# Optimization experiments

Hardware: AMD Instinct MI355X
Metric: run time of the kernel (lower is better)

The kernel has to match this reference:

```python
import jax, jax.numpy as jnp
import numpy as np

HID = 128          # args.hid
HEADS = 1          # args.head (forced: concat=True and classifier expects 3*hid)
C = HID            # out_channels per head
ND, NPR, NCL = 4096, 20000, 1024
E_DD, E_DP, E_CP = 500_000, 1_000_000, 500_000
B = 8192
SLOPE = 0.2        # GATConv negative_slope default


def _gat(x_src, x_dst, src, dst, W, a_src, a_dst, bias, num_dst,
         edge_attr=None, W_edge=None, a_edge=None):
    # PyG GATConv: shared lin for src/dst (in_channels is int)
    hs = (x_src @ W).reshape(-1, HEADS, C)            # [Ns,H,C]
    hd = (x_dst @ W).reshape(-1, HEADS, C)            # [Nd,H,C]
    e = jnp.sum(hs * a_src, -1)[src] + jnp.sum(hd * a_dst, -1)[dst]  # [E,H]
    if edge_attr is not None:
        ee = (edge_attr @ W_edge).reshape(-1, HEADS, C)
        e = e + jnp.sum(ee * a_edge, -1)
    e = jnp.where(e > 0, e, SLOPE * e)                # leaky_relu
    emax = jax.ops.segment_max(e, dst, num_segments=num_dst)
    ex = jnp.exp(e - emax[dst])
    denom = jax.ops.segment_sum(ex, dst, num_segments=num_dst)
    alpha = ex / (denom[dst] + 1e-16)                 # PyG softmax eps
    out = jax.ops.segment_sum(hs[src] * alpha[:, :, None], dst, num_segments=num_dst)
    return out.reshape(num_dst, HEADS * C) + bias


def _l2n(x):
    return x / jnp.maximum(jnp.linalg.norm(x, axis=1, keepdims=True), 1e-12)


def setup_inputs() -> dict:
    key = jax.random.key(0)
    ks = iter(jax.random.split(key, 48))

    def nrm(shape, s=0.1):
        return jax.random.normal(next(ks), shape, jnp.float32) * s

    inp = {
        'x_drug': jnp.arange(ND, dtype=jnp.int32),
        'x_protein': jnp.arange(NPR, dtype=jnp.int32),
        'x_cell': jnp.arange(NCL, dtype=jnp.int32),
        'ei_dd': jax.random.randint(next(ks), (2, E_DD), 0, ND),
        'edge_attr_dd': jax.random.normal(next(ks), (E_DD, 1), jnp.float32),
        'src_dp': jax.random.randint(next(ks), (E_DP,), 0, NPR),
        'dst_dp': jax.random.randint(next(ks), (E_DP,), 0, ND),
        'src_cp': jax.random.randint(next(ks), (E_CP,), 0, NPR),
        'dst_cp': jax.random.randint(next(ks), (E_CP,), 0, NCL),
        'drug1': jax.random.randint(next(ks), (B,), 0, ND),
        'drug2': jax.random.randint(next(ks), (B,), 0, ND),
        'cell': jax.random.randint(next(ks), (B,), 0, NCL),
        # embedding tables
        'drug_emb': nrm((ND, HID), 1.0),
        'protein_emb': nrm((NPR, HID), 1.0),
        'cell_emb': nrm((NCL, HID), 1.0),
        # GAT d-d (edge_dim=1)
        'W_dd': nrm((HID, HEADS * C)), 'a_src_dd': nrm((HEADS, C)), 'a_dst_dd': nrm((HEADS, C)),
        'bias_dd': jnp.zeros((HEADS * C,), jnp.float32),
        'W_edge_dd': nrm((1, HEADS * C)), 'a_edge_dd': nrm((HEADS, C)),
        # GAT protein->drug
        'W_dp': nrm((HID, HEADS * C)), 'a_src_dp': nrm((HEADS, C)), 'a_dst_dp': nrm((HEADS, C)),
        'bias_dp': jnp.zeros((HEADS * C,), jnp.float32),
        # GAT protein->cell
        'W_cp': nrm((HID, HEADS * C)), 'a_src_cp': nrm((HEADS, C)), 'a_dst_cp': nrm((HEADS, C)),
        'bias_cp': jnp.zeros((HEADS * C,), jnp.float32),
        # classifier: 3h -> 6h -> 2h -> 2
        'W1': nrm((3 * HID, 6 * HID)), 'b1': jnp.zeros((6 * HID,), jnp.float32),
        'W2': nrm((6 * HID, 2 * HID)), 'b2': jnp.zeros((2 * HID,), jnp.float32),
        'W3': nrm((2 * HID, 2)), 'b3': jnp.zeros((2,), jnp.float32),
    }
    return inp


def reference(x_drug, x_protein, x_cell, ei_dd, edge_attr_dd, src_dp, dst_dp,
              src_cp, dst_cp, drug1, drug2, cell, drug_emb, protein_emb, cell_emb,
              W_dd, a_src_dd, a_dst_dd, bias_dd, W_edge_dd, a_edge_dd,
              W_dp, a_src_dp, a_dst_dp, bias_dp,
              W_cp, a_src_cp, a_dst_cp, bias_cp,
              W1, b1, W2, b2, W3, b3):
    h_d = drug_emb[x_drug]
    h_p = protein_emb[x_protein]
    h_c = cell_emb[x_cell]

    # d-d: add self-loops with edge_attr fill_value='mean' (PyG default)
    src, dst = ei_dd[0], ei_dd[1]
    deg = jax.ops.segment_sum(jnp.ones((E_DD,), jnp.float32), dst, num_segments=ND)
    mean_attr = jax.ops.segment_sum(edge_attr_dd, dst, num_segments=ND) / jnp.maximum(deg, 1.0)[:, None]
    loops = jnp.arange(ND, dtype=src.dtype)
    src2 = jnp.concatenate([src, loops])
    dst2 = jnp.concatenate([dst, loops])
    attr2 = jnp.concatenate([edge_attr_dd, mean_attr], 0)

    out_dd = _gat(h_d, h_d, src2, dst2, W_dd, a_src_dd, a_dst_dd, bias_dd, ND,
                  attr2, W_edge_dd, a_edge_dd)
    out_dp = _gat(h_p, h_d, src_dp, dst_dp, W_dp, a_src_dp, a_dst_dp, bias_dp, ND)
    out_cp = _gat(h_p, h_c, src_cp, dst_cp, W_cp, a_src_cp, a_dst_cp, bias_cp, NCL)

    drug = jax.nn.relu(out_dd + out_dp)   # HeteroConv aggr='sum', then F.relu
    cellx = jax.nn.relu(out_cp)

    hid = jnp.concatenate([_l2n(drug[drug1]), _l2n(drug[drug2]), _l2n(cellx[cell])], 1)
    h = jax.nn.relu(hid @ W1 + b1)        # dropout = identity in eval
    h = jax.nn.relu(h @ W2 + b2)
    return h @ W3 + b3
```

## Files before the change

### kernel.cpp

```cpp
#include <hip/hip_runtime.h>
#include <hip/hip_bf16.h>

#define HIDC 128
typedef __hip_bfloat16 bf16;
typedef __attribute__((ext_vector_type(8))) short short8;
typedef __attribute__((ext_vector_type(4))) float floatx4;

#define CHUNK 4096

__device__ __forceinline__ short f2b(float f) {
    unsigned int u = __builtin_bit_cast(unsigned int, f);
    u += 0x7fff + ((u >> 16) & 1);
    return (short)(u >> 16);
}

__device__ __forceinline__ uint packe(int s, float ev) {
    float w = __expf(ev);
    return ((uint)s << 16) | (uint)(unsigned short)f2b(w);
}

__global__ void __launch_bounds__(256) r11_prep(
    int* __restrict__ zptr, int zwords, int nzb,
    const float* __restrict__ W_dd, const float* __restrict__ W_dp, const float* __restrict__ W_cp,
    const float* __restrict__ a0, const float* __restrict__ a1, const float* __restrict__ a2,
    const float* __restrict__ a3, const float* __restrict__ a4, const float* __restrict__ a5,
    const float* __restrict__ W_edge, const float* __restrict__ a_edge,
    float* __restrict__ wa, float* __restrict__ c_edge,
    const float* __restrict__ W1, short* __restrict__ Wt1, int nT1,
    const float* __restrict__ W2, short* __restrict__ Wt2)
{
    int b = blockIdx.x;
    int tid = threadIdx.x;
    if (b < nzb) {
        int i = b * 256 + tid;
        if (i < zwords) zptr[i] = 0;
        return;
    }
    b -= nzb;
    if (b < 7) {
        __shared__ float as[HIDC];
        int k = tid;
        if (b < 6) {
            const float* W = (b < 2) ? W_dd : (b < 4) ? W_dp : W_cp;
            const float* a = (b == 0) ? a0 : (b == 1) ? a1 : (b == 2) ? a2 : (b == 3) ? a3 : (b == 4) ? a4 : a5;
            if (k < HIDC) as[k] = a[k];
            __syncthreads();
            if (k < HIDC) {
                float s = 0.f;
#pragma unroll 8
                for (int c = 0; c < HIDC; c++) s = fmaf(W[k * HIDC + c], as[c], s);
                wa[b * HIDC + k] = s;
            }
        } else {
            if (k < HIDC) as[k] = W_edge[k] * a_edge[k];
            __syncthreads();
#pragma unroll
            for (int off = 64; off > 0; off >>= 1) { if (k < off) as[k] += as[k + off]; __syncthreads(); }
            if (k == 0) c_edge[0] = as[0];
        }
        return;
    }
    b -= 7;
    const float* W; short* Wt; int K, N, k0, n0;
    if (b < nT1) { W = W1; Wt = Wt1; K = 384; N = 768; k0 = (b / 24) * 32; n0 = (b % 24) * 32; }
    else { b -= nT1; W = W2; Wt = Wt2; K = 768; N = 256; k0 = (b / 8) * 32; n0 = (b % 8) * 32; }
    __shared__ short T[32 * 34];
    int cc = tid & 31, rr = tid >> 5;
#pragma unroll
    for (int it = 0; it < 4; it++) {
        int r = it * 8 + rr;
        T[r * 34 + cc] = f2b(W[(size_t)(k0 + r) * N + n0 + cc]);
    }
    __syncthreads();
#pragma unroll
    for (int it = 0; it < 4; it++) {
        int r = it * 8 + rr;
        Wt[(size_t)(n0 + r) * K + k0 + cc] = T[cc * 34 + r];
    }
}

__global__ void __launch_bounds__(256) r11_scalars(
    const float* __restrict__ drug_emb, const float* __restrict__ prot_emb, const float* __restrict__ cell_emb,
    const int* __restrict__ x_drug, const int* __restrict__ x_prot, const int* __restrict__ x_cell,
    const float* __restrict__ wa,
    float* __restrict__ ssrc_dd, float* __restrict__ sdst_dd, float* __restrict__ sdst_dp,
    float* __restrict__ ssrc_dp, float* __restrict__ ssrc_cp, float* __restrict__ sdst_cp,
    int nd, int npr, int ncl)
{
    int g = blockIdx.x * 4 + (threadIdx.x >> 6);
    int l = threadIdx.x & 63;
    const float2* wa2 = (const float2*)wa;
    if (g < nd) {
        int id = x_drug[g];
        float2 e = ((const float2*)drug_emb)[(size_t)id * 64 + l];
        float2 w0 = wa2[0 * 64 + l], w1 = wa2[1 * 64 + l], w3 = wa2[3 * 64 + l];
        float p0 = e.x * w0.x + e.y * w0.y;
        float p1 = e.x * w1.x + e.y * w1.y;
        float p2 = e.x * w3.x + e.y * w3.y;
#pragma unroll
        for (int off = 32; off > 0; off >>= 1) {
            p0 += __shfl_xor(p0, off, 64);
            p1 += __shfl_xor(p1, off, 64);
            p2 += __shfl_xor(p2, off, 64);
        }
        if (l == 0) { ssrc_dd[g] = p0; sdst_dd[g] = p1; sdst_dp[g] = p2; }
    } else if (g < nd + npr) {
        int r = g - nd;
        int id = x_prot[r];
        float2 e = ((const float2*)prot_emb)[(size_t)id * 64 + l];
        float2 w2 = wa2[2 * 64 + l], w4 = wa2[4 * 64 + l];
        float p0 = e.x * w2.x + e.y * w2.y;
        float p1 = e.x * w4.x + e.y * w4.y;
#pragma unroll
        for (int off = 32; off > 0; off >>= 1) {
            p0 += __shfl_xor(p0, off, 64);
            p1 += __shfl_xor(p1, off, 64);
        }
        if (l == 0) { ssrc_dp[r] = p0; ssrc_cp[r] = p1; }
    } else if (g < nd + npr + ncl) {
        int r = g - nd - npr;
        int id = x_cell[r];
        float2 e = ((const float2*)cell_emb)[(size_t)id * 64 + l];
        float2 w5 = wa2[5 * 64 + l];
        float p0 = e.x * w5.x + e.y * w5.y;
#pragma unroll
        for (int off = 32; off > 0; off >>= 1) p0 += __shfl_xor(p0, off, 64);
        if (l == 0) sdst_cp[r] = p0;
    }
}

__global__ void __launch_bounds__(128) r11_node_gemm(
    const float* __restrict__ drug_emb, const int* __restrict__ x_drug,
    const float* __restrict__ W_dd, bf16* __restrict__ H_dd, int ndb,
    const float* __restrict__ prot_emb, const int* __restrict__ x_prot,
    const float* __restrict__ W_dp, const float* __restrict__ W_cp,
    bf16* __restrict__ H_dp, bf16* __restrict__ H_cp)
{
    __shared__ int ids[16];
    __shared__ float xs[16 * HIDC];
    int bb = blockIdx.x;
    bool isdrug = bb < ndb;
    int r0 = (isdrug ? bb : bb - ndb) * 16;
    const float* emb = isdrug ? drug_emb : prot_emb;
    const int* idx = isdrug ? x_drug : x_prot;
    int tid = threadIdx.x;
    if (tid < 16) ids[tid] = idx[r0 + tid];
    __syncthreads();
    for (int t = tid; t < 16 * HIDC; t += 128) {
        int r = t >> 7, k = t & 127;
        xs[t] = emb[(size_t)ids[r] * HIDC + k];
    }
    __syncthreads();
    int c = tid;
    if (isdrug) {
        float acc[16];
#pragma unroll
        for (int r = 0; r < 16; r++) acc[r] = 0.f;
        for (int k = 0; k < HIDC; k += 4) {
            float w0 = W_dd[(k + 0) * HIDC + c];
            float w1 = W_dd[(k + 1) * HIDC + c];
            float w2 = W_dd[(k + 2) * HIDC + c];
            float w3 = W_dd[(k + 3) * HIDC + c];
#pragma unroll
            for (int r = 0; r < 16; r++) {
                float4 x = *(const float4*)&xs[r * HIDC + k];
                acc[r] = fmaf(x.x, w0, fmaf(x.y, w1, fmaf(x.z, w2, fmaf(x.w, w3, acc[r]))));
            }
        }
#pragma unroll
        for (int r = 0; r < 16; r++) H_dd[(size_t)(r0 + r) * HIDC + c] = __float2bfloat16(acc[r]);
    } else {
        float accA[16], accB[16];
#pragma unroll
        for (int r = 0; r < 16; r++) { accA[r] = 0.f; accB[r] = 0.f; }
        for (int k = 0; k < HIDC; k += 2) {
            float a0 = W_dp[(k + 0) * HIDC + c];
            float a1 = W_dp[(k + 1) * HIDC + c];
            float b0 = W_cp[(k + 0) * HIDC + c];
            float b1 = W_cp[(k + 1) * HIDC + c];
#pragma unroll
            for (int r = 0; r < 16; r++) {
                float2 x = *(const float2*)&xs[r * HIDC + k];
                accA[r] = fmaf(x.x, a0, fmaf(x.y, a1, accA[r]));
                accB[r] = fmaf(x.x, b0, fmaf(x.y, b1, accB[r]));
            }
        }
#pragma unroll
        for (int r = 0; r < 16; r++) {
            H_dp[(size_t)(r0 + r) * HIDC + c] = __float2bfloat16(accA[r]);
            H_cp[(size_t)(r0 + r) * HIDC + c] = __float2bfloat16(accB[r]);
        }
    }
}

__global__ void __launch_bounds__(256) r11_edge_pass1(
    const int* __restrict__ dst_dd, const float* __restrict__ attr_dd, int E_dd, int nb_dd,
    const int* __restrict__ dst_dp, int E_dp, int nb_dp,
    const int* __restrict__ dst_cp, int E_cp,
    int nd, int ncl,
    int* __restrict__ cnt_dd, float* __restrict__ attr_sum,
    int* __restrict__ cnt_dp, int* __restrict__ cnt_cp,
    int* __restrict__ rank_dd, int* __restrict__ rank_dp, int* __restrict__ rank_cp)
{
    __shared__ int lcnt[4096];
    __shared__ float lattr[4096];
    int bid = blockIdx.x;
    const int* dst; const float* attr = nullptr; int E, e0, bins;
    int* gcnt; int* rank;
    if (bid < nb_dd) {
        dst = dst_dd; attr = attr_dd; E = E_dd; e0 = bid * CHUNK; bins = nd;
        gcnt = cnt_dd; rank = rank_dd;
    } else if (bid < nb_dd + nb_dp) {
        dst = dst_dp; E = E_dp; e0 = (bid - nb_dd) * CHUNK; bins = nd;
        gcnt = cnt_dp; rank = rank_dp;
    } else {
        dst = dst_cp; E = E_cp; e0 = (bid - nb_dd - nb_dp) * CHUNK; bins = ncl;
        gcnt = cnt_cp; rank = rank_cp;
    }
    int tid = threadIdx.x;
    for (int b = tid; b < bins; b += 256) { lcnt[b] = 0; if (attr) lattr[b] = 0.f; }
    __syncthreads();
    int e1 = min(e0 + CHUNK, E);
    for (int i = e0 + tid; i < e1; i += 256) {
        int d = dst[i];
        rank[i] = atomicAdd(&lcnt[d], 1);
        if (attr) atomicAdd(&lattr[d], attr[i]);
    }
    __syncthreads();
    for (int b = tid; b < bins; b += 256) {
        int c = lcnt[b];
        if (c > 0) {
            lcnt[b] = atomicAdd(&gcnt[b], c);
            if (attr) atomicAdd(&attr_sum[b], lattr[b]);
        }
    }
    __syncthreads();
    for (int i = e0 + tid; i < e1; i += 256) {
        rank[i] += lcnt[dst[i]];
    }
}

__global__ void __launch_bounds__(1024) r11_exscan3(
    const int* __restrict__ in0, int* __restrict__ out0, int n0,
    const int* __restrict__ in1, int* __restrict__ out1, int n1,
    const int* __restrict__ in2, int* __restrict__ out2, int n2)
{
    const int* in; int* out; int n; int inc;
    if (blockIdx.x == 0)      { in = in0; out = out0; n = n0; inc = 1; }
    else if (blockIdx.x == 1) { in = in1; out = out1; n = n1; inc = 0; }
    else                      { in = in2; out = out2; n = n2; inc = 0; }
    __shared__ int buf[1024];
    __shared__ int carry;
    int tid = threadIdx.x;
    if (tid == 0) carry = 0;
    __syncthreads();
    for (int base = 0; base < n; base += 1024) {
        int i = base + tid;
        int v = (i < n) ? (in[i] + inc) : 0;
        buf[tid] = v; __syncthreads();
        for (int off = 1; off < 1024; off <<= 1) {
            int t = (tid >= off) ? buf[tid - off] : 0;
            __syncthreads();
            buf[tid] += t;
            __syncthreads();
        }
        int c0 = carry;
        int incl = buf[tid];
        if (i < n) out[i] = c0 + incl - v;
        __syncthreads();
        if (tid == 1023) carry = c0 + buf[1023];
        __syncthreads();
    }
    if (tid == 0) out[n] = carry;
}

__global__ void r11_scatter(
    const int* __restrict__ ei_dd, const float* __restrict__ attr_dd, int E_dd, int nd,
    const int* __restrict__ src_dp, const int* __restrict__ dst_dp, int E_dp,
    const int* __restrict__ src_cp, const int* __restrict__ dst_cp, int E_cp,
    const int* __restrict__ rank_dd, const int* __restrict__ rank_dp, const int* __restrict__ rank_cp,
    const int* __restrict__ deg_dd, const float* __restrict__ attr_sum,
    const float* __restrict__ c_edge_ptr,
    const float* __restrict__ ssrc_dd, const float* __restrict__ sdst_dd,
    const float* __restrict__ ssrc_dp, const float* __restrict__ sdst_dp,
    const float* __restrict__ ssrc_cp, const float* __restrict__ sdst_cp,
    const int* __restrict__ rs_dd, const int* __restrict__ rs_dp, const int* __restrict__ rs_cp,
    uint* __restrict__ csr_dd, uint* __restrict__ csr_dp, uint* __restrict__ csr_cp)
{
    int i = blockIdx.x * 256 + threadIdx.x;
    if (i < E_dd) {
        int s = ei_dd[i], d = ei_dd[E_dd + i];
        float ev = ssrc_dd[s] + sdst_dd[d] + attr_dd[i] * c_edge_ptr[0];
        ev = (ev > 0.f) ? ev : 0.2f * ev;
        csr_dd[rs_dd[d] + rank_dd[i]] = packe(s, ev);
        return;
    }
    i -= E_dd;
    if (i < nd) {
        int d = i;
        int dg = deg_dd[d];
        float mean = attr_sum[d] / fmaxf((float)dg, 1.0f);
        float ev = ssrc_dd[d] + sdst_dd[d] + mean * c_edge_ptr[0];
        ev = (ev > 0.f) ? ev : 0.2f * ev;
        csr_dd[rs_dd[d] + dg] = packe(d, ev);
        return;
    }
    i -= nd;
    if (i < E_dp) {
        int d = dst_dp[i], s = src_dp[i];
        float ev = ssrc_dp[s] + sdst_dp[d];
        ev = (ev > 0.f) ? ev : 0.2f * ev;
        csr_dp[rs_dp[d] + rank_dp[i]] = packe(s, ev);
        return;
    }
    i -= E_dp;
    if (i < E_cp) {
        int d = dst_cp[i], s = src_cp[i];
        float ev = ssrc_cp[s] + sdst_cp[d];
        ev = (ev > 0.f) ? ev : 0.2f * ev;
        csr_cp[rs_cp[d] + rank_cp[i]] = packe(s, ev);
    }
}

__global__ void __launch_bounds__(64) r11_agg3(
    const int* __restrict__ rs_dd, const uint* __restrict__ csr_dd, const uint* __restrict__ Hdd,
    float* __restrict__ agg_dd, int nd,
    const int* __restrict__ rs_dp, const uint* __restrict__ csr_dp, const uint* __restrict__ Hdp,
    float* __restrict__ agg_dp,
    const int* __restrict__ rs_cp, const uint* __restrict__ csr_cp, const uint* __restrict__ Hcp,
    float* __restrict__ agg_cp, int R)
{
    int b = blockIdx.x;
    int slot = b & 7;
    int half = slot >> 2;
    int row_g = (b >> 3) * 4 + (slot & 3);
    if (row_g >= R) return;
    const int* rs; const uint* csr; const uint* H2; float* out; int row;
    if (row_g < nd)          { rs = rs_dd; csr = csr_dd; H2 = Hdd; out = agg_dd; row = row_g; }
    else if (row_g < 2 * nd) { rs = rs_dp; csr = csr_dp; H2 = Hdp; out = agg_dp; row = row_g - nd; }
    else                     { rs = rs_cp; csr = csr_cp; H2 = Hcp; out = agg_cp; row = row_g - 2 * nd; }
    int t = threadIdx.x;
    int c = t & 31, g = t >> 5;
    int s = rs[row], e = rs[row + 1];

    float sum = 0.f;
    for (int i = s + t; i < e; i += 64) sum += __uint_as_float((csr[i] & 0xffffu) << 16);
#pragma unroll
    for (int off = 32; off > 0; off >>= 1) sum += __shfl_xor(sum, off, 64);
    float inv = 1.f / (sum + 1e-16f);

    __shared__ float se[64];
    __shared__ int ss[64];
    const uint* Hh = H2 + half * 32 + c;
    float accx = 0.f, accy = 0.f;
    int base = s;
    for (; base + 64 <= e; base += 64) {
        uint pk = csr[base + t];
        se[t] = __uint_as_float((pk & 0xffffu) << 16);
        ss[t] = (int)(pk >> 16);
        __syncthreads();
#pragma unroll 8
        for (int jj = 0; jj < 32; jj++) {
            int j = jj * 2 + g;
            uint u = Hh[(size_t)ss[j] * 64];
            float w = se[j];
            accx = fmaf(w, __uint_as_float(u << 16), accx);
            accy = fmaf(w, __uint_as_float(u & 0xffff0000u), accy);
        }
        __syncthreads();
    }
    if (base < e) {
        int lim = e - base;
        if (t < lim) {
            uint pk = csr[base + t];
            se[t] = __uint_as_float((pk & 0xffffu) << 16);
            ss[t] = (int)(pk >> 16);
        }
        __syncthreads();
        for (int j = g; j < lim; j += 2) {
            uint u = Hh[(size_t)ss[j] * 64];
            float w = se[j];
            accx = fmaf(w, __uint_as_float(u << 16), accx);
            accy = fmaf(w, __uint_as_float(u & 0xffff0000u), accy);
        }
        __syncthreads();
    }
    accx += __shfl_xor(accx, 32, 64);
    accy += __shfl_xor(accy, 32, 64);
    if (t < 32) {
        float2 o; o.x = accx * inv; o.y = accy * inv;
        ((float2*)out)[(size_t)row * 64 + half * 32 + c] = o;
    }
}

__global__ void __launch_bounds__(128) r11_fuse(
    const float* __restrict__ agg_dd, const float* __restrict__ bias_dd,
    const float* __restrict__ agg_dp, const float* __restrict__ bias_dp,
    float* __restrict__ drugN, int nd,
    const float* __restrict__ agg_cp, const float* __restrict__ bias_cp,
    float* __restrict__ cellN)
{
    int b = blockIdx.x, c = threadIdx.x;
    float v;
    float* outN;
    int d;
    if (b < nd) {
        d = b;
        v = agg_dd[(size_t)d * HIDC + c] + bias_dd[c] + agg_dp[(size_t)d * HIDC + c] + bias_dp[c];
        outN = drugN;
    } else {
        d = b - nd;
        v = agg_cp[(size_t)d * HIDC + c] + bias_cp[c];
        outN = cellN;
    }
    v = fmaxf(v, 0.f);
    __shared__ float red[HIDC];
    red[c] = v * v; __syncthreads();
#pragma unroll
    for (int off = 64; off > 0; off >>= 1) { if (c < off) red[c] += red[c + off]; __syncthreads(); }
    float nrm = fmaxf(sqrtf(red[0]), 1e-12f);
    outN[(size_t)d * HIDC + c] = v / nrm;
}

__global__ void __launch_bounds__(128) r11_gather_hid(
    const float* __restrict__ drugN, const float* __restrict__ cellN,
    const int* __restrict__ d1, const int* __restrict__ d2, const int* __restrict__ ce,
    short* __restrict__ hid)
{
    int b = blockIdx.x, c = threadIdx.x;
    hid[(size_t)b * 384 + c]       = f2b(drugN[(size_t)d1[b] * HIDC + c]);
    hid[(size_t)b * 384 + 128 + c] = f2b(drugN[(size_t)d2[b] * HIDC + c]);
    hid[(size_t)b * 384 + 256 + c] = f2b(cellN[(size_t)ce[b] * HIDC + c]);
}

template <int NB, int OUT_BF16>
__global__ void __launch_bounds__(256) r11_mgemm(
    const short* __restrict__ X, const short* __restrict__ Wt, const float* __restrict__ bias,
    void* __restrict__ Y, int M, int K, int N)
{
    constexpr int BN = NB * 16;
    __shared__ short As[128 * 40];
    __shared__ short Bs[BN * 40];
    int m0 = blockIdx.x * 128, n0 = blockIdx.y * BN;
    int tid = threadIdx.x;
    int w = tid >> 6, lane = tid & 63;
    int q = lane >> 4, t = lane & 15;
    int sr = tid >> 1, sc = tid & 1;

    floatx4 acc[2][NB];
#pragma unroll
    for (int i = 0; i < 2; i++)
#pragma unroll
        for (int c = 0; c < NB; c++) acc[i][c] = (floatx4){0.f, 0.f, 0.f, 0.f};

    for (int kt = 0; kt < K; kt += 32) {
        {
            const uint4* ga = (const uint4*)(X + (size_t)(m0 + sr) * K + kt + sc * 16);
            uint4 a0 = ga[0], a1 = ga[1];
            *(uint4*)&As[sr * 40 + sc * 16]     = a0;
            *(uint4*)&As[sr * 40 + sc * 16 + 8] = a1;
        }
        for (int tt = tid; tt < BN * 2; tt += 256) {
            int r = tt >> 1, h = tt & 1;
            const uint4* gb = (const uint4*)(Wt + (size_t)(n0 + r) * K + kt + h * 16);
            uint4 b0 = gb[0], b1 = gb[1];
            *(uint4*)&Bs[r * 40 + h * 16]     = b0;
            *(uint4*)&Bs[r * 40 + h * 16 + 8] = b1;
        }
        __syncthreads();
        short8 af[2], bf[NB];
#pragma unroll
        for (int i = 0; i < 2; i++)
            af[i] = *(const short8*)&As[(w * 32 + i * 16 + t) * 40 + q * 8];
#pragma unroll
        for (int c = 0; c < NB; c++)
            bf[c] = *(const short8*)&Bs[(c * 16 + t) * 40 + q * 8];
#pragma unroll
        for (int i = 0; i < 2; i++)
#pragma unroll
            for (int c = 0; c < NB; c++)
                acc[i][c] = __builtin_amdgcn_mfma_f32_16x16x32_bf16(af[i], bf[c], acc[i][c], 0, 0, 0);
        __syncthreads();
    }

    float bv[NB];
#pragma unroll
    for (int c = 0; c < NB; c++) bv[c] = bias[n0 + c * 16 + t];
#pragma unroll
    for (int i = 0; i < 2; i++) {
#pragma unroll
        for (int c = 0; c < NB; c++) {
#pragma unroll
            for (int ii = 0; ii < 4; ii++) {
                int m_g = m0 + w * 32 + i * 16 + q * 4 + ii;
                int n_g = n0 + c * 16 + t;
                float v = acc[i][c][ii] + bv[c];
                v = fmaxf(v, 0.f);
                if (OUT_BF16) ((short*)Y)[(size_t)m_g * N + n_g] = f2b(v);
                else          ((float*)Y)[(size_t)m_g * N + n_g] = v;
            }
        }
    }
}

__global__ void __launch_bounds__(256) r11_final(
    const float* __restrict__ h2, const float* __restrict__ W3, const float* __restrict__ b3,
    float* __restrict__ out)
{
    int row = blockIdx.x * 4 + (threadIdx.x >> 6);
    int lane = threadIdx.x & 63;
    float a0 = 0.f, a1 = 0.f;
    for (int k = lane; k < 256; k += 64) {
        float h = h2[(size_t)row * 256 + k];
        a0 = fmaf(h, W3[k * 2 + 0], a0);
        a1 = fmaf(h, W3[k * 2 + 1], a1);
    }
#pragma unroll
    for (int off = 32; off > 0; off >>= 1) {
        a0 += __shfl_down(a0, off, 64);
        a1 += __shfl_down(a1, off, 64);
    }
    if (lane == 0) {
        out[row * 2 + 0] = a0 + b3[0];
        out[row * 2 + 1] = a1 + b3[1];
    }
}

extern "C" void kernel_launch(void* const* d_in, const int* in_sizes, int n_in,
                              void* d_out, int out_size, void* d_ws, size_t ws_size,
                              hipStream_t stream)
{
    const int* x_drug      = (const int*)d_in[0];
    const int* x_protein   = (const int*)d_in[1];
    const int* x_cell      = (const int*)d_in[2];
    const int* ei_dd       = (const int*)d_in[3];
    const float* attr_dd   = (const float*)d_in[4];
    const int* src_dp      = (const int*)d_in[5];
    const int* dst_dp      = (const int*)d_in[6];
    const int* src_cp      = (const int*)d_in[7];
    const int* dst_cp      = (const int*)d_in[8];
    const int* drug1       = (const int*)d_in[9];
    const int* drug2       = (const int*)d_in[10];
    const int* cellb       = (const int*)d_in[11];
    const float* drug_emb  = (const float*)d_in[12];
    const float* protein_emb = (const float*)d_in[13];
    const float* cell_emb  = (const float*)d_in[14];
    const float* W_dd      = (const float*)d_in[15];
    const float* a_src_dd  = (const float*)d_in[16];
    const float* a_dst_dd  = (const float*)d_in[17];
    const float* bias_dd   = (const float*)d_in[18];
    const float* W_edge_dd = (const float*)d_in[19];
    const float* a_edge_dd = (const float*)d_in[20];
    const float* W_dp      = (const float*)d_in[21];
    const float* a_src_dp  = (const float*)d_in[22];
    const float* a_dst_dp  = (const float*)d_in[23];
    const float* bias_dp   = (const float*)d_in[24];
    const float* W_cp      = (const float*)d_in[25];
    const float* a_src_cp  = (const float*)d_in[26];
    const float* a_dst_cp  = (const float*)d_in[27];
    const float* bias_cp   = (const float*)d_in[28];
    const float* W1        = (const float*)d_in[29];
    const float* b1        = (const float*)d_in[30];
    const float* W2        = (const float*)d_in[31];
    const float* b2        = (const float*)d_in[32];
    const float* W3        = (const float*)d_in[33];
    const float* b3        = (const float*)d_in[34];

    const int ND  = in_sizes[0];
    const int NPR = in_sizes[1];
    const int NCL = in_sizes[2];
    const int E_DD = in_sizes[4];
    const int E_DP = in_sizes[5];
    const int E_CP = in_sizes[7];
    const int B    = in_sizes[9];
    const int E_DD2 = E_DD + ND;

    char* p = (char*)d_ws;
    auto carve = [&](size_t bytes) -> char* {
        char* r = p;
        p += (bytes + 255) & ~(size_t)255;
        return r;
    };
    char* zstart = p;
    int*   cnt_dd   = (int*)  carve((size_t)ND * 4);
    float* attr_sum = (float*)carve((size_t)ND * 4);
    int*   cnt_dp   = (int*)  carve((size_t)ND * 4);
    int*   cnt_cp   = (int*)  carve((size_t)NCL * 4);
    size_t zbytes = (size_t)(p - zstart);
    int*   rs_dd    = (int*)  carve((size_t)(ND + 1) * 4);
    int*   rs_dp    = (int*)  carve((size_t)(ND + 1) * 4);
    int*   rs_cp    = (int*)  carve((size_t)(NCL + 1) * 4);
    float* c_edge   = (float*)carve(256);
    float* wa       = (float*)carve(6 * HIDC * 4);
    bf16*  H_dd     = (bf16*) carve((size_t)ND * HIDC * 2);
    bf16*  H_dp     = (bf16*) carve((size_t)NPR * HIDC * 2);
    bf16*  H_cp     = (bf16*) carve((size_t)NPR * HIDC * 2);
    float* ssrc_dd  = (float*)carve((size_t)ND * 4);
    float* sdst_dd  = (float*)carve((size_t)ND * 4);
    float* ssrc_dp  = (float*)carve((size_t)NPR * 4);
    float* sdst_dp  = (float*)carve((size_t)ND * 4);
    float* ssrc_cp  = (float*)carve((size_t)NPR * 4);
    float* sdst_cp  = (float*)carve((size_t)NCL * 4);
    int*   rank_dd  = (int*)  carve((size_t)E_DD * 4);
    int*   rank_dp  = (int*)  carve((size_t)E_DP * 4);
    int*   rank_cp  = (int*)  carve((size_t)E_CP * 4);
    uint*  csr_dd   = (uint*) carve((size_t)E_DD2 * 4);
    uint*  csr_dp   = (uint*) carve((size_t)E_DP * 4);
    uint*  csr_cp   = (uint*) carve((size_t)E_CP * 4);
    float* agg_dd   = (float*)carve((size_t)ND * HIDC * 4);
    float* agg_dp   = (float*)carve((size_t)ND * HIDC * 4);
    float* agg_cp   = (float*)carve((size_t)NCL * HIDC * 4);
    float* drugN    = (float*)carve((size_t)ND * HIDC * 4);
    float* cellN    = (float*)carve((size_t)NCL * HIDC * 4);
    short* hidb     = (short*)carve((size_t)B * 384 * 2);
    short* h1b      = (short*)carve((size_t)B * 768 * 2);
    float* h2       = (float*)carve((size_t)B * 256 * 4);
    short* Wt1      = (short*)carve((size_t)384 * 768 * 2);
    short* Wt2      = (short*)carve((size_t)768 * 256 * 2);

    auto cdiv = [](int a, int b) { return (a + b - 1) / b; };

    int zwords = (int)(zbytes / 4);
    int nzb = cdiv(zwords, 256);
    int nT1 = (384 / 32) * (768 / 32);
    int nT2 = (768 / 32) * (256 / 32);
    r11_prep<<<nzb + 7 + nT1 + nT2, 256, 0, stream>>>(
        (int*)zstart, zwords, nzb,
        W_dd, W_dp, W_cp, a_src_dd, a_dst_dd, a_src_dp, a_dst_dp, a_src_cp, a_dst_cp,
        W_edge_dd, a_edge_dd, wa, c_edge, W1, Wt1, nT1, W2, Wt2);

    r11_node_gemm<<<ND / 16 + NPR / 16, 128, 0, stream>>>(
        drug_emb, x_drug, W_dd, H_dd, ND / 16,
        protein_emb, x_protein, W_dp, W_cp, H_dp, H_cp);
    r11_scalars<<<(ND + NPR + NCL) / 4, 256, 0, stream>>>(
        drug_emb, protein_emb, cell_emb, x_drug, x_protein, x_cell, wa,
        ssrc_dd, sdst_dd, sdst_dp, ssrc_dp, ssrc_cp, sdst_cp, ND, NPR, NCL);

    int nb_dd = cdiv(E_DD, CHUNK), nb_dp = cdiv(E_DP, CHUNK), nb_cp = cdiv(E_CP, CHUNK);
    r11_edge_pass1<<<nb_dd + nb_dp + nb_cp, 256, 0, stream>>>(
        ei_dd + E_DD, attr_dd, E_DD, nb_dd,
        dst_dp, E_DP, nb_dp,
        dst_cp, E_CP,
        ND, NCL,
        cnt_dd, attr_sum, cnt_dp, cnt_cp, rank_dd, rank_dp, rank_cp);
    r11_exscan3<<<3, 1024, 0, stream>>>(cnt_dd, rs_dd, ND, cnt_dp, rs_dp, ND, cnt_cp, rs_cp, NCL);
    r11_scatter<<<cdiv(E_DD + ND + E_DP + E_CP, 256), 256, 0, stream>>>(
        ei_dd, attr_dd, E_DD, ND, src_dp, dst_dp, E_DP, src_cp, dst_cp, E_CP,
        rank_dd, rank_dp, rank_cp, cnt_dd, attr_sum, c_edge,
        ssrc_dd, sdst_dd, ssrc_dp, sdst_dp, ssrc_cp, sdst_cp,
        rs_dd, rs_dp, rs_cp, csr_dd, csr_dp, csr_cp);

    {
        int R = 2 * ND + NCL;
        int G = cdiv(R, 4) * 8;
        r11_agg3<<<G, 64, 0, stream>>>(
            rs_dd, csr_dd, (const uint*)H_dd, agg_dd, ND,
            rs_dp, csr_dp, (const uint*)H_dp, agg_dp,
            rs_cp, csr_cp, (const uint*)H_cp, agg_cp, R);
    }

    r11_fuse<<<ND + NCL, 128, 0, stream>>>(agg_dd, bias_dd, agg_dp, bias_dp, drugN, ND,
                                           agg_cp, bias_cp, cellN);

    r11_gather_hid<<<B, 128, 0, stream>>>(drugN, cellN, drug1, drug2, cellb, hidb);
    {
        dim3 g1(B / 128, 768 / 128);
        r11_mgemm<8, 1><<<g1, 256, 0, stream>>>(hidb, Wt1, b1, (void*)h1b, B, 384, 768);
        dim3 g2(B / 128, 256 / 64);
        r11_mgemm<4, 0><<<g2, 256, 0, stream>>>(h1b, Wt2, b2, (void*)h2, B, 768, 256);
    }
    r11_final<<<B / 4, 256, 0, stream>>>(h2, W3, b3, (float*)d_out);
}
```

Baseline: 340.3 us.

## Drop global rank arrays via cursor-based chunked scatter; widen aggregation blocks

The CSR build no longer writes and reads back per-edge rank arrays. Pass1 now only counts, the scan also initialises per-bin cursors, and the scatter recomputes local ranks in shared memory per chunk and reserves slots with atomics on those cursors. The aggregation kernel goes from 64 to 256 threads per row group, with a shared-memory reduction for the softmax denominator and for the partial accumulators. This removes rank-array traffic and gives more parallelism per row, at the cost of an extra shared-memory atomic pass in the scatter and more block synchronisation in the aggregation.

```diff
diff --git a/kernel.cpp b/kernel.cpp
--- a/kernel.cpp
+++ b/kernel.cpp
@@ -19,7 +19,7 @@
     return ((uint)s << 16) | (uint)(unsigned short)f2b(w);
 }
 
-__global__ void __launch_bounds__(256) r11_prep(
+__global__ void __launch_bounds__(256) r12_prep(
     int* __restrict__ zptr, int zwords, int nzb,
     const float* __restrict__ W_dd, const float* __restrict__ W_dp, const float* __restrict__ W_cp,
     const float* __restrict__ a0, const float* __restrict__ a1, const float* __restrict__ a2,
@@ -79,7 +79,7 @@
     }
 }
 
-__global__ void __launch_bounds__(256) r11_scalars(
+__global__ void __launch_bounds__(256) r12_scalars(
     const float* __restrict__ drug_emb, const float* __restrict__ prot_emb, const float* __restrict__ cell_emb,
     const int* __restrict__ x_drug, const int* __restrict__ x_prot, const int* __restrict__ x_cell,
     const float* __restrict__ wa,
@@ -129,7 +129,7 @@
     }
 }
 
-__global__ void __launch_bounds__(128) r11_node_gemm(
+__global__ void __launch_bounds__(128) r12_node_gemm(
     const float* __restrict__ drug_emb, const int* __restrict__ x_drug,
     const float* __restrict__ W_dd, bf16* __restrict__ H_dd, int ndb,
     const float* __restrict__ prot_emb, const int* __restrict__ x_prot,
@@ -193,29 +193,25 @@
     }
 }
 
-__global__ void __launch_bounds__(256) r11_edge_pass1(
+__global__ void __launch_bounds__(256) r12_pass1(
     const int* __restrict__ dst_dd, const float* __restrict__ attr_dd, int E_dd, int nb_dd,
     const int* __restrict__ dst_dp, int E_dp, int nb_dp,
     const int* __restrict__ dst_cp, int E_cp,
     int nd, int ncl,
     int* __restrict__ cnt_dd, float* __restrict__ attr_sum,
-    int* __restrict__ cnt_dp, int* __restrict__ cnt_cp,
-    int* __restrict__ rank_dd, int* __restrict__ rank_dp, int* __restrict__ rank_cp)
+    int* __restrict__ cnt_dp, int* __restrict__ cnt_cp)
 {
     __shared__ int lcnt[4096];
     __shared__ float lattr[4096];
     int bid = blockIdx.x;
     const int* dst; const float* attr = nullptr; int E, e0, bins;
-    int* gcnt; int* rank;
+    int* gcnt;
     if (bid < nb_dd) {
-        dst = dst_dd; attr = attr_dd; E = E_dd; e0 = bid * CHUNK; bins = nd;
-        gcnt = cnt_dd; rank = rank_dd;
+        dst = dst_dd; attr = attr_dd; E = E_dd; e0 = bid * CHUNK; bins = nd; gcnt = cnt_dd;
     } else if (bid < nb_dd + nb_dp) {
-        dst = dst_dp; E = E_dp; e0 = (bid - nb_dd) * CHUNK; bins = nd;
-        gcnt = cnt_dp; rank = rank_dp;
+        dst = dst_dp; E = E_dp; e0 = (bid - nb_dd) * CHUNK; bins = nd; gcnt = cnt_dp;
     } else {
-        dst = dst_cp; E = E_cp; e0 = (bid - nb_dd - nb_dp) * CHUNK; bins = ncl;
-        gcnt = cnt_cp; rank = rank_cp;
+        dst = dst_cp; E = E_cp; e0 = (bid - nb_dd - nb_dp) * CHUNK; bins = ncl; gcnt = cnt_cp;
     }
     int tid = threadIdx.x;
     for (int b = tid; b < bins; b += 256) { lcnt[b] = 0; if (attr) lattr[b] = 0.f; }
@@ -223,32 +219,28 @@
     int e1 = min(e0 + CHUNK, E);
     for (int i = e0 + tid; i < e1; i += 256) {
         int d = dst[i];
-        rank[i] = atomicAdd(&lcnt[d], 1);
+        atomicAdd(&lcnt[d], 1);
         if (attr) atomicAdd(&lattr[d], attr[i]);
     }
     __syncthreads();
     for (int b = tid; b < bins; b += 256) {
         int c = lcnt[b];
         if (c > 0) {
-            lcnt[b] = atomicAdd(&gcnt[b], c);
+            atomicAdd(&gcnt[b], c);
             if (attr) atomicAdd(&attr_sum[b], lattr[b]);
         }
     }
-    __syncthreads();
-    for (int i = e0 + tid; i < e1; i += 256) {
-        rank[i] += lcnt[dst[i]];
-    }
-}
-
-__global__ void __launch_bounds__(1024) r11_exscan3(
-    const int* __restrict__ in0, int* __restrict__ out0, int n0,
-    const int* __restrict__ in1, int* __restrict__ out1, int n1,
-    const int* __restrict__ in2, int* __restrict__ out2, int n2)
-{
-    const int* in; int* out; int n; int inc;
-    if (blockIdx.x == 0)      { in = in0; out = out0; n = n0; inc = 1; }
-    else if (blockIdx.x == 1) { in = in1; out = out1; n = n1; inc = 0; }
-    else                      { in = in2; out = out2; n = n2; inc = 0; }
+}
+
+__global__ void __launch_bounds__(1024) r12_exscan3(
+    const int* __restrict__ in0, int* __restrict__ out0, int* __restrict__ cur0, int n0,
+    const int* __restrict__ in1, int* __restrict__ out1, int* __restrict__ cur1, int n1,
+    const int* __restrict__ in2, int* __restrict__ out2, int* __restrict__ cur2, int n2)
+{
+    const int* in; int* out; int* cur; int n; int inc;
+    if (blockIdx.x == 0)      { in = in0; out = out0; cur = cur0; n = n0; inc = 1; }
+    else if (blockIdx.x == 1) { in = in1; out = out1; cur = cur1; n = n1; inc = 0; }
+    else                      { in = in2; out = out2; cur = cur2; n = n2; inc = 0; }
     __shared__ int buf[1024];
     __shared__ int carry;
     int tid = threadIdx.x;
@@ -266,7 +258,7 @@
         }
         int c0 = carry;
         int incl = buf[tid];
-        if (i < n) out[i] = c0 + incl - v;
+        if (i < n) { int r = c0 + incl - v; out[i] = r; cur[i] = r; }
         __syncthreads();
         if (tid == 1023) carry = c0 + buf[1023];
         __syncthreads();
@@ -274,55 +266,75 @@
     if (tid == 0) out[n] = carry;
 }
 
-__global__ void r11_scatter(
-    const int* __restrict__ ei_dd, const float* __restrict__ attr_dd, int E_dd, int nd,
-    const int* __restrict__ src_dp, const int* __restrict__ dst_dp, int E_dp,
-    const int* __restrict__ src_cp, const int* __restrict__ dst_cp, int E_cp,
-    const int* __restrict__ rank_dd, const int* __restrict__ rank_dp, const int* __restrict__ rank_cp,
-    const int* __restrict__ deg_dd, const float* __restrict__ attr_sum,
+__global__ void __launch_bounds__(256) r12_scatter(
+    const int* __restrict__ ei_dd, const float* __restrict__ attr_dd, int E_dd, int nb_dd, int nd,
+    const int* __restrict__ src_dp, const int* __restrict__ dst_dp, int E_dp, int nb_dp,
+    const int* __restrict__ src_cp, const int* __restrict__ dst_cp, int E_cp, int nb_cp, int ncl,
+    const int* __restrict__ cnt_dd, const float* __restrict__ attr_sum,
     const float* __restrict__ c_edge_ptr,
     const float* __restrict__ ssrc_dd, const float* __restrict__ sdst_dd,
     const float* __restrict__ ssrc_dp, const float* __restrict__ sdst_dp,
     const float* __restrict__ ssrc_cp, const float* __restrict__ sdst_cp,
-    const int* __restrict__ rs_dd, const int* __restrict__ rs_dp, const int* __restrict__ rs_cp,
+    int* __restrict__ cur_dd, int* __restrict__ cur_dp, int* __restrict__ cur_cp,
     uint* __restrict__ csr_dd, uint* __restrict__ csr_dp, uint* __restrict__ csr_cp)
 {
-    int i = blockIdx.x * 256 + threadIdx.x;
-    if (i < E_dd) {
-        int s = ei_dd[i], d = ei_dd[E_dd + i];
-        float ev = ssrc_dd[s] + sdst_dd[d] + attr_dd[i] * c_edge_ptr[0];
-        ev = (ev > 0.f) ? ev : 0.2f * ev;
-        csr_dd[rs_dd[d] + rank_dd[i]] = packe(s, ev);
-        return;
-    }
-    i -= E_dd;
-    if (i < nd) {
-        int d = i;
-        int dg = deg_dd[d];
+    __shared__ int lcnt[4096];
+    int bid = blockIdx.x;
+    int tid = threadIdx.x;
+    int nbe = nb_dd + nb_dp + nb_cp;
+    if (bid >= nbe) {
+        int d = (bid - nbe) * 256 + tid;
+        if (d >= nd) return;
+        int dg = cnt_dd[d];
         float mean = attr_sum[d] / fmaxf((float)dg, 1.0f);
         float ev = ssrc_dd[d] + sdst_dd[d] + mean * c_edge_ptr[0];
         ev = (ev > 0.f) ? ev : 0.2f * ev;
-        csr_dd[rs_dd[d] + dg] = packe(d, ev);
+        int slot = atomicAdd(&cur_dd[d], 1);
+        csr_dd[slot] = packe(d, ev);
         return;
     }
-    i -= nd;
-    if (i < E_dp) {
-        int d = dst_dp[i], s = src_dp[i];
-        float ev = ssrc_dp[s] + sdst_dp[d];
-        ev = (ev > 0.f) ? ev : 0.2f * ev;
-        csr_dp[rs_dp[d] + rank_dp[i]] = packe(s, ev);
-        return;
-    }
-    i -= E_dp;
-    if (i < E_cp) {
-        int d = dst_cp[i], s = src_cp[i];
-        float ev = ssrc_cp[s] + sdst_cp[d];
-        ev = (ev > 0.f) ? ev : 0.2f * ev;
-        csr_cp[rs_cp[d] + rank_cp[i]] = packe(s, ev);
-    }
-}
-
-__global__ void __launch_bounds__(64) r11_agg3(
+    const int *srcp, *dstp; const float* attr = nullptr; int E, e0, bins;
+    int* cur; uint* csr; const float *ssrc, *sdst;
+    if (bid < nb_dd) {
+        srcp = ei_dd; dstp = ei_dd + E_dd; attr = attr_dd; E = E_dd; e0 = bid * CHUNK;
+        bins = nd; cur = cur_dd; csr = csr_dd; ssrc = ssrc_dd; sdst = sdst_dd;
+    } else if (bid < nb_dd + nb_dp) {
+        srcp = src_dp; dstp = dst_dp; E = E_dp; e0 = (bid - nb_dd) * CHUNK;
+        bins = nd; cur = cur_dp; csr = csr_dp; ssrc = ssrc_dp; sdst = sdst_dp;
+    } else {
+        srcp = src_cp; dstp = dst_cp; E = E_cp; e0 = (bid - nb_dd - nb_dp) * CHUNK;
+        bins = ncl; cur = cur_cp; csr = csr_cp; ssrc = ssrc_cp; sdst = sdst_cp;
+    }
+    for (int b = tid; b < bins; b += 256) lcnt[b] = 0;
+    __syncthreads();
+    int e1 = min(e0 + CHUNK, E);
+    int lr[16];
+#pragma unroll
+    for (int k = 0; k < 16; k++) {
+        int i = e0 + k * 256 + tid;
+        if (i < e1) lr[k] = atomicAdd(&lcnt[dstp[i]], 1);
+    }
+    __syncthreads();
+    for (int b = tid; b < bins; b += 256) {
+        int c = lcnt[b];
+        if (c > 0) lcnt[b] = atomicAdd(&cur[b], c);
+    }
+    __syncthreads();
+    float ce = c_edge_ptr[0];
+#pragma unroll
+    for (int k = 0; k < 16; k++) {
+        int i = e0 + k * 256 + tid;
+        if (i < e1) {
+            int d = dstp[i], s = srcp[i];
+            float ev = ssrc[s] + sdst[d];
+            if (attr) ev += attr[i] * ce;
+            ev = (ev > 0.f) ? ev : 0.2f * ev;
+            csr[lcnt[d] + lr[k]] = packe(s, ev);
+        }
+    }
+}
+
+__global__ void __launch_bounds__(256) r12_agg3(
     const int* __restrict__ rs_dd, const uint* __restrict__ csr_dd, const uint* __restrict__ Hdd,
     float* __restrict__ agg_dd, int nd,
     const int* __restrict__ rs_dp, const uint* __restrict__ csr_dp, const uint* __restrict__ Hdp,
@@ -343,11 +355,16 @@
     int c = t & 31, g = t >> 5;
     int s = rs[row], e = rs[row + 1];
 
+    __shared__ float red[256];
     float sum = 0.f;
-    for (int i = s + t; i < e; i += 64) sum += __uint_as_float((csr[i] & 0xffffu) << 16);
-#pragma unroll
-    for (int off = 32; off > 0; off >>= 1) sum += __shfl_xor(sum, off, 64);
-    float inv = 1.f / (sum + 1e-16f);
+    for (int i = s + t; i < e; i += 256) sum += __uint_as_float((csr[i] & 0xffffu) << 16);
+    red[t] = sum; __syncthreads();
+#pragma unroll
+    for (int off = 128; off > 0; off >>= 1) {
+        if (t < off) red[t] += red[t + off];
+        __syncthreads();
+    }
+    float inv = 1.f / (red[0] + 1e-16f);
 
     __shared__ float se[64];
     __shared__ int ss[64];
@@ -355,13 +372,15 @@
     float accx = 0.f, accy = 0.f;
     int base = s;
     for (; base + 64 <= e; base += 64) {
-        uint pk = csr[base + t];
-        se[t] = __uint_as_float((pk & 0xffffu) << 16);
-        ss[t] = (int)(pk >> 16);
+        if (t < 64) {
+            uint pk = csr[base + t];
+            se[t] = __uint_as_float((pk & 0xffffu) << 16);
+            ss[t] = (int)(pk >> 16);
+        }
         __syncthreads();
 #pragma unroll 8
-        for (int jj = 0; jj < 32; jj++) {
-            int j = jj * 2 + g;
+        for (int jj = 0; jj < 8; jj++) {
+            int j = jj * 8 + g;
             uint u = Hh[(size_t)ss[j] * 64];
             float w = se[j];
             accx = fmaf(w, __uint_as_float(u << 16), accx);
@@ -377,7 +396,7 @@
             ss[t] = (int)(pk >> 16);
         }
         __syncthreads();
-        for (int j = g; j < lim; j += 2) {
+        for (int j = g; j < lim; j += 8) {
             uint u = Hh[(size_t)ss[j] * 64];
             float w = se[j];
             accx = fmaf(w, __uint_as_float(u << 16), accx);
@@ -387,13 +406,20 @@
     }
     accx += __shfl_xor(accx, 32, 64);
     accy += __shfl_xor(accy, 32, 64);
+    __shared__ float rx[128], ry[128];
+    int w = t >> 6, l = t & 63;
+    if (l < 32) { rx[w * 32 + c] = accx; ry[w * 32 + c] = accy; }
+    __syncthreads();
     if (t < 32) {
-        float2 o; o.x = accx * inv; o.y = accy * inv;
-        ((float2*)out)[(size_t)row * 64 + half * 32 + c] = o;
-    }
-}
-
-__global__ void __launch_bounds__(128) r11_fuse(
+        float ax = 0.f, ay = 0.f;
+#pragma unroll
+        for (int ww = 0; ww < 4; ww++) { ax += rx[ww * 32 + t]; ay += ry[ww * 32 + t]; }
+        float2 o; o.x = ax * inv; o.y = ay * inv;
+        ((float2*)out)[(size_t)row * 64 + half * 32 + t] = o;
+    }
+}
+
+__global__ void __launch_bounds__(128) r12_fuse(
     const float* __restrict__ agg_dd, const float* __restrict__ bias_dd,
     const float* __restrict__ agg_dp, const float* __restrict__ bias_dp,
     float* __restrict__ drugN, int nd,
@@ -422,7 +448,7 @@
     outN[(size_t)d * HIDC + c] = v / nrm;
 }
 
-__global__ void __launch_bounds__(128) r11_gather_hid(
+__global__ void __launch_bounds__(128) r12_gather_hid(
     const float* __restrict__ drugN, const float* __restrict__ cellN,
     const int* __restrict__ d1, const int* __restrict__ d2, const int* __restrict__ ce,
     short* __restrict__ hid)
@@ -434,7 +460,7 @@
 }
 
 template <int NB, int OUT_BF16>
-__global__ void __launch_bounds__(256) r11_mgemm(
+__global__ void __launch_bounds__(256) r12_mgemm(
     const short* __restrict__ X, const short* __restrict__ Wt, const float* __restrict__ bias,
     void* __restrict__ Y, int M, int K, int N)
 {
@@ -503,7 +529,7 @@
     }
 }
 
-__global__ void __launch_bounds__(256) r11_final(
+__global__ void __launch_bounds__(256) r12_final(
     const float* __restrict__ h2, const float* __restrict__ W3, const float* __restrict__ b3,
     float* __restrict__ out)
 {
@@ -590,6 +616,9 @@
     int*   rs_dd    = (int*)  carve((size_t)(ND + 1) * 4);
     int*   rs_dp    = (int*)  carve((size_t)(ND + 1) * 4);
     int*   rs_cp    = (int*)  carve((size_t)(NCL + 1) * 4);
+    int*   cur_dd   = (int*)  carve((size_t)ND * 4);
+    int*   cur_dp   = (int*)  carve((size_t)ND * 4);
+    int*   cur_cp   = (int*)  carve((size_t)NCL * 4);
     float* c_edge   = (float*)carve(256);
     float* wa       = (float*)carve(6 * HIDC * 4);
     bf16*  H_dd     = (bf16*) carve((size_t)ND * HIDC * 2);
@@ -601,9 +630,6 @@
     float* sdst_dp  = (float*)carve((size_t)ND * 4);
     float* ssrc_cp  = (float*)carve((size_t)NPR * 4);
     float* sdst_cp  = (float*)carve((size_t)NCL * 4);
-    int*   rank_dd  = (int*)  carve((size_t)E_DD * 4);
-    int*   rank_dp  = (int*)  carve((size_t)E_DP * 4);
-    int*   rank_cp  = (int*)  carve((size_t)E_CP * 4);
     uint*  csr_dd   = (uint*) carve((size_t)E_DD2 * 4);
     uint*  csr_dp   = (uint*) carve((size_t)E_DP * 4);
     uint*  csr_cp   = (uint*) carve((size_t)E_CP * 4);
@@ -624,50 +650,54 @@
     int nzb = cdiv(zwords, 256);
     int nT1 = (384 / 32) * (768 / 32);
     int nT2 = (768 / 32) * (256 / 32);
-    r11_prep<<<nzb + 7 + nT1 + nT2, 256, 0, stream>>>(
+    r12_prep<<<nzb + 7 + nT1 + nT2, 256, 0, stream>>>(
         (int*)zstart, zwords, nzb,
         W_dd, W_dp, W_cp, a_src_dd, a_dst_dd, a_src_dp, a_dst_dp, a_src_cp, a_dst_cp,
         W_edge_dd, a_edge_dd, wa, c_edge, W1, Wt1, nT1, W2, Wt2);
 
-    r11_node_gemm<<<ND / 16 + NPR / 16, 128, 0, stream>>>(
+    r12_node_gemm<<<ND / 16 + NPR / 16, 128, 0, stream>>>(
         drug_emb, x_drug, W_dd, H_dd, ND / 16,
         protein_emb, x_protein, W_dp, W_cp, H_dp, H_cp);
-    r11_scalars<<<(ND + NPR + NCL) / 4, 256, 0, stream>>>(
+    r12_scalars<<<(ND + NPR + NCL) / 4, 256, 0, stream>>>(
         drug_emb, protein_emb, cell_emb, x_drug, x_protein, x_cell, wa,
         ssrc_dd, sdst_dd, sdst_dp, ssrc_dp, ssrc_cp, sdst_cp, ND, NPR, NCL);
 
     int nb_dd = cdiv(E_DD, CHUNK), nb_dp = cdiv(E_DP, CHUNK), nb_cp = cdiv(E_CP, CHUNK);
-    r11_edge_pass1<<<nb_dd + nb_dp + nb_cp, 256, 0, stream>>>(
+    r12_pass1<<<nb_dd + nb_dp + nb_cp, 256, 0, stream>>>(
         ei_dd + E_DD, attr_dd, E_DD, nb_dd,
         dst_dp, E_DP, nb_dp,
         dst_cp, E_CP,
         ND, NCL,
-        cnt_dd, attr_sum, cnt_dp, cnt_cp, rank_dd, rank_dp, rank_cp);
-    r11_exscan3<<<3, 1024, 0, stream>>>(cnt_dd, rs_dd, ND, cnt_dp, rs_dp, ND, cnt_cp, rs_cp, NCL);
-    r11_scatter<<<cdiv(E_DD + ND + E_DP + E_CP, 256), 256, 0, stream>>>(
-        ei_dd, attr_dd, E_DD, ND, src_dp, dst_dp, E_DP, src_cp, dst_cp, E_CP,
-        rank_dd, rank_dp, rank_cp, cnt_dd, attr_sum, c_edge,
+        cnt_dd, attr_sum, cnt_dp, cnt_cp);
+    r12_exscan3<<<3, 1024, 0, stream>>>(cnt_dd, rs_dd, cur_dd, ND,
+                                        cnt_dp, rs_dp, cur_dp, ND,
+                                        cnt_cp, rs_cp, cur_cp, NCL);
+    r12_scatter<<<nb_dd + nb_dp + nb_cp + cdiv(ND, 256), 256, 0, stream>>>(
+        ei_dd, attr_dd, E_DD, nb_dd, ND,
+        src_dp, dst_dp, E_DP, nb_dp,
+        src_cp, dst_cp, E_CP, nb_cp, NCL,
+        cnt_dd, attr_sum, c_edge,
         ssrc_dd, sdst_dd, ssrc_dp, sdst_dp, ssrc_cp, sdst_cp,
-        rs_dd, rs_dp, rs_cp, csr_dd, csr_dp, csr_cp);
+        cur_dd, cur_dp, cur_cp, csr_dd, csr_dp, csr_cp);
 
     {
         int R = 2 * ND + NCL;
         int G = cdiv(R, 4) * 8;
-        r11_agg3<<<G, 64, 0, stream>>>(
+        r12_agg3<<<G, 256, 0, stream>>>(
             rs_dd, csr_dd, (const uint*)H_dd, agg_dd, ND,
             rs_dp, csr_dp, (const uint*)H_dp, agg_dp,
             rs_cp, csr_cp, (const uint*)H_cp, agg_cp, R);
     }
 
-    r11_fuse<<<ND + NCL, 128, 0, stream>>>(agg_dd, bias_dd, agg_dp, bias_dp, drugN, ND,
+    r12_fuse<<<ND + NCL, 128, 0, stream>>>(agg_dd, bias_dd, agg_dp, bias_dp, drugN, ND,
                                            agg_cp, bias_cp, cellN);
 
-    r11_gather_hid<<<B, 128, 0, stream>>>(drugN, cellN, drug1, drug2, cellb, hidb);
+    r12_gather_hid<<<B, 128, 0, stream>>>(drugN, cellN, drug1, drug2, cellb, hidb);
     {
         dim3 g1(B / 128, 768 / 128);
-        r11_mgemm<8, 1><<<g1, 256, 0, stream>>>(hidb, Wt1, b1, (void*)h1b, B, 384, 768);
+        r12_mgemm<8, 1><<<g1, 256, 0, stream>>>(hidb, Wt1, b1, (void*)h1b, B, 384, 768);
         dim3 g2(B / 128, 256 / 64);
-        r11_mgemm<4, 0><<<g2, 256, 0, stream>>>(h1b, Wt2, b2, (void*)h2, B, 768, 256);
-    }
-    r11_final<<<B / 4, 256, 0, stream>>>(h2, W3, b3, (float*)d_out);
-}
+        r12_mgemm<4, 0><<<g2, 256, 0, stream>>>(h1b, Wt2, b2, (void*)h2, B, 768, 256);
+    }
+    r12_final<<<B / 4, 256, 0, stream>>>(h2, W3, b3, (float*)d_out);
+}
```

After: 348.2 us. 2.3% more time.
